# Kernel optimization log

Hardware: AMD Instinct MI355X
Metric: run time of the kernel (lower is better)

The kernel has to match this reference:

```python
import jax, jax.numpy as jnp
import numpy as np
import math

N, CIN, DM, H, W = 4, 64, 32, 64, 64
KH = KW = 3

def setup_inputs() -> dict:
    key = jax.random.key(0)
    ks = jax.random.split(key, 12)
    sc = 0.05
    return {
        "h": jax.random.normal(ks[0], (N, CIN, H, W), jnp.float32),
        "m": jax.random.normal(ks[1], (N, CIN, H, W), jnp.float32),
        "Wh": jax.random.normal(ks[2], (3 * DM, CIN), jnp.float32) * sc,
        "bh": jax.random.normal(ks[3], (3 * DM,), jnp.float32) * sc,
        "Wm": jax.random.normal(ks[4], (2 * DM, CIN), jnp.float32) * sc,
        "bm": jax.random.normal(ks[5], (2 * DM,), jnp.float32) * sc,
        "Wz": jax.random.normal(ks[6], (DM, 2 * DM), jnp.float32) * sc,
        "bz": jax.random.normal(ks[7], (DM,), jnp.float32) * sc,
        "Wo": jax.random.normal(ks[8], (3 * CIN, CIN + DM, KH, KW), jnp.float32) * sc,
        "bo": jax.random.normal(ks[9], (3 * CIN,), jnp.float32) * sc,
    }

def _conv1x1(x, Wt, b):
    # x: [N,Ci,H,W], Wt: [Co,Ci] -> [N,Co,H,W]
    return jnp.einsum('oi,nihw->nohw', Wt, x) + b[None, :, None, None]

def _attend(q, k, v):
    # q,k,v: [N,C,S]; out: [N,C,S]
    C = q.shape[1]
    scores = jnp.einsum('ncs,nct->nst', q, k) / math.sqrt(C)  # [N,S,S]
    attn = jax.nn.softmax(scores, axis=-1)
    return jnp.einsum('nst,nct->ncs', attn, v)

def reference(h, m, Wh, bh, Wm, bm, Wz, bz, Wo, bo):
    n, _, hh, ww = h.shape
    S = hh * ww
    hq, hk, hv = jnp.split(_conv1x1(h, Wh, bh), 3, axis=1)
    mk, mv = jnp.split(_conv1x1(m, Wm, bm), 2, axis=1)
    hq = hq.reshape(n, DM, S)
    hk = hk.reshape(n, DM, S)
    hv = hv.reshape(n, DM, S)
    mk = mk.reshape(n, DM, S)
    mv = mv.reshape(n, DM, S)
    Zh = _attend(hq, hk, hv).reshape(n, DM, hh, ww)
    Zm = _attend(hq, mk, mv).reshape(n, DM, hh, ww)
    Z = _conv1x1(jnp.concatenate([Zh, Zm], axis=1), Wz, bz)
    x = jnp.concatenate([Z, h], axis=1)  # [N, DM+CIN, H, W]
    out = jax.lax.conv_general_dilated(
        x, Wo, window_strides=(1, 1), padding='SAME',
        dimension_numbers=('NCHW', 'OIHW', 'NCHW')) + bo[None, :, None, None]
    i, g, o = jnp.split(out, 3, axis=1)
    i = jax.nn.sigmoid(i)
    g = jnp.tanh(g)
    m_next = i * g + (1.0 - i) * m
    h_next = jax.nn.sigmoid(o) * m_next
    return (h_next, m_next)
```

## Files before the change

### kernel.cpp

```cpp
#include <hip/hip_runtime.h>
#include <math.h>

#define NB 4
#define CIN 64
#define DM 32
#define S 4096
#define NW 8

#define OFF_Q  0
#define OFF_KH 262144
#define OFF_VH 524288
#define OFF_KM 786432
#define OFF_VM 1048576
#define OFF_ZH 1310720
#define OFF_ZM 1572864
#define OFF_WF 1835008

typedef __attribute__((ext_vector_type(8))) short bf16x8;
typedef __attribute__((ext_vector_type(4))) short s16x4;
typedef __attribute__((ext_vector_type(4))) float f32x4;

__device__ inline unsigned short f2b(float x) {
  union { float f; unsigned u; } v;
  v.f = x;
  unsigned r = (v.u + 0x7FFF + ((v.u >> 16) & 1)) >> 16;
  return (unsigned short)r;
}

__device__ inline float b2f(unsigned short u) {
  union { unsigned u; float f; } v;
  v.u = ((unsigned)u) << 16;
  return v.f;
}

__global__ __launch_bounds__(256) void prep_kernel(
    const float* __restrict__ h, const float* __restrict__ m,
    const float* __restrict__ Wh, const float* __restrict__ bh,
    const float* __restrict__ Wm, const float* __restrict__ bm,
    const float* __restrict__ Wo, float* __restrict__ ws) {
  __shared__ float lin[64][64];
  __shared__ unsigned short sm[64][34];
  int bid = blockIdx.x;
  int tid = threadIdx.x;

  if (bid >= 512) {
    int idx = (bid - 512) * 256 + tid;
    int co = idx / 432;
    int rem = idx - co * 432;
    int tap = rem / 48;
    int cp = rem - tap * 48;
    int ci0 = cp * 2;
    float a = Wo[((size_t)co * 96 + ci0) * 9 + tap];
    float b = Wo[((size_t)co * 96 + ci0 + 1) * 9 + tap];
    unsigned val = (unsigned)f2b(a) | ((unsigned)f2b(b) << 16);
    ((unsigned*)(ws + OFF_WF))[idx] = val;
    return;
  }

  int mode = (bid >= 256) ? 1 : 0;
  const float* in = mode ? m : h;
  const float* W = mode ? Wm : Wh;
  const float* b = mode ? bm : bh;
  int lbid = bid & 255;
  int n = lbid >> 6;
  int s0 = (lbid & 63) * 64;
  int sl = tid & 63;
  int cg = tid >> 6;
  const float* inp = in + (size_t)n * CIN * S + s0;
#pragma unroll
  for (int r = 0; r < 16; ++r) {
    int ci = r * 4 + cg;
    lin[ci][sl] = inp[(size_t)ci * S + sl];
  }
  __syncthreads();
  int na = (mode == 0) ? 24 : 16;
  float acc[24];
  for (int k = 0; k < na; ++k) {
    int co = cg + k * 4;
    const float* w = W + co * CIN;
    float a = b[co];
#pragma unroll
    for (int ci = 0; ci < CIN; ++ci) a += w[ci] * lin[ci][sl];
    acc[k] = a;
  }

  unsigned short* qsl = (unsigned short*)(ws + OFF_Q);
  unsigned short* khs = (unsigned short*)(ws + OFF_KH);
  unsigned short* vhs = (unsigned short*)(ws + OFF_VH);
  unsigned short* kms = (unsigned short*)(ws + OFF_KM);
  unsigned short* vms = (unsigned short*)(ws + OFF_VM);

  int ngrp = (mode == 0) ? 2 : 1;
  for (int g = 0; g < ngrp; ++g) {
    __syncthreads();
    const float rs = 0.17677669529663687f;
#pragma unroll
    for (int j = 0; j < 8; ++j) {
      int k = g * 8 + j;
      int c = cg + 4 * j;
      float v = acc[k];
      if (mode == 0 && g == 0) v *= rs;
      sm[sl][c] = f2b(v);
    }
    __syncthreads();
    unsigned short* dst;
    if (mode == 0)
      dst = (g == 0 ? qsl : khs);
    else
      dst = kms;
    unsigned* du = (unsigned*)(dst + ((size_t)n * S + s0) * 32);
#pragma unroll
    for (int i = 0; i < 4; ++i) {
      int idx = tid + i * 256;
      int s = idx >> 4, cp = idx & 15;
      unsigned val = (unsigned)sm[s][2 * cp] | ((unsigned)sm[s][2 * cp + 1] << 16);
      du[idx] = val;
    }
  }
  int k0 = (mode == 0) ? 16 : 8;
  unsigned short* vdst = (mode == 0) ? vhs : vms;
#pragma unroll
  for (int j = 0; j < 8; ++j) {
    int k = k0 + j;
    int c = cg + 4 * j;
    vdst[((size_t)n * DM + c) * S + s0 + sl] = f2b(acc[k]);
  }
}

union AttnSmem {
  unsigned short P[NW][2][16][76];
  struct {
    float osh[NW][2][32][16];
    float lsh[NW][2][16];
    unsigned short Olds[2][16][40];
  } e;
};

__global__ __launch_bounds__(512, 4) void attn_kernel(
    float* __restrict__ ws, const float* __restrict__ Wz,
    const float* __restrict__ bz) {
  __shared__ AttnSmem sm;

  int bid = blockIdx.x;
  int ph = bid & 1;
  int n = (bid >> 1) & 3;
  int q0 = (bid >> 3) * 32;
  int tid = threadIdx.x;
  int w = tid >> 6;
  int lane = tid & 63;
  int ql = lane & 15;
  int quad = lane >> 4;
  int kbase = w * 512;

  const unsigned short* qs = (const unsigned short*)(ws + OFF_Q) + ((size_t)n * S + q0) * 32;
  const unsigned short* Ks = (const unsigned short*)(ws + (ph ? OFF_KM : OFF_KH)) + (size_t)n * S * 32;
  const unsigned short* Vs = (const unsigned short*)(ws + (ph ? OFF_VM : OFF_VH)) + (size_t)n * DM * S;
  unsigned short* Zp = (unsigned short*)(ws + (ph ? OFF_ZM : OFF_ZH)) + (size_t)n * DM * S;

  bf16x8 qf0 = *(const bf16x8*)(qs + ql * 32 + quad * 8);
  bf16x8 qf1 = *(const bf16x8*)(qs + (16 + ql) * 32 + quad * 8);

  f32x4 o00 = {0.f, 0.f, 0.f, 0.f}, o01 = {0.f, 0.f, 0.f, 0.f};
  f32x4 o10 = {0.f, 0.f, 0.f, 0.f}, o11 = {0.f, 0.f, 0.f, 0.f};
  float lrun0 = 0.f, lrun1 = 0.f;
  const f32x4 zinit = {-8.f, -8.f, -8.f, -8.f};

  bf16x8 kf[4], kfn[4], vf[4];
#pragma unroll
  for (int t = 0; t < 4; ++t)
    kf[t] = *(const bf16x8*)(Ks + (size_t)(kbase + t * 16 + ql) * 32 + quad * 8);

  for (int it = 0; it < 8; ++it) {
    int kb = kbase + it * 64;
    int kbn = kbase + ((it + 1) & 7) * 64;
#pragma unroll
    for (int c2 = 0; c2 < 2; ++c2)
#pragma unroll
      for (int t2 = 0; t2 < 2; ++t2)
        vf[c2 * 2 + t2] = *(const bf16x8*)(Vs + (size_t)(t2 * 16 + ql) * S + kb + c2 * 32 + quad * 8);
#pragma unroll
    for (int t = 0; t < 4; ++t)
      kfn[t] = *(const bf16x8*)(Ks + (size_t)(kbn + t * 16 + ql) * 32 + quad * 8);

    float ls0 = 0.f;
#pragma unroll
    for (int t = 0; t < 4; ++t) {
      f32x4 stt = __builtin_amdgcn_mfma_f32_16x16x32_bf16(kf[t], qf0, zinit, 0, 0, 0);
      s16x4 pp;
#pragma unroll
      for (int r = 0; r < 4; ++r) {
        float p = __expf(stt[r]);
        ls0 += p;
        pp[r] = (short)f2b(p);
      }
      *(s16x4*)(&sm.P[w][0][ql][t * 16 + quad * 4]) = pp;
    }
    lrun0 += ls0;
    float ls1 = 0.f;
#pragma unroll
    for (int t = 0; t < 4; ++t) {
      f32x4 stt = __builtin_amdgcn_mfma_f32_16x16x32_bf16(kf[t], qf1, zinit, 0, 0, 0);
      s16x4 pp;
#pragma unroll
      for (int r = 0; r < 4; ++r) {
        float p = __expf(stt[r]);
        ls1 += p;
        pp[r] = (short)f2b(p);
      }
      *(s16x4*)(&sm.P[w][1][ql][t * 16 + quad * 4]) = pp;
    }
    lrun1 += ls1;

    __builtin_amdgcn_s_waitcnt(0xC07F);
    __builtin_amdgcn_wave_barrier();

#pragma unroll
    for (int c2 = 0; c2 < 2; ++c2) {
      bf16x8 pf0 = *(const bf16x8*)(&sm.P[w][0][ql][c2 * 32 + quad * 8]);
      bf16x8 pf1 = *(const bf16x8*)(&sm.P[w][1][ql][c2 * 32 + quad * 8]);
      o00 = __builtin_amdgcn_mfma_f32_16x16x32_bf16(vf[c2 * 2 + 0], pf0, o00, 0, 0, 0);
      o01 = __builtin_amdgcn_mfma_f32_16x16x32_bf16(vf[c2 * 2 + 1], pf0, o01, 0, 0, 0);
      o10 = __builtin_amdgcn_mfma_f32_16x16x32_bf16(vf[c2 * 2 + 0], pf1, o10, 0, 0, 0);
      o11 = __builtin_amdgcn_mfma_f32_16x16x32_bf16(vf[c2 * 2 + 1], pf1, o11, 0, 0, 0);
    }
    __builtin_amdgcn_wave_barrier();

#pragma unroll
    for (int t = 0; t < 4; ++t) kf[t] = kfn[t];
  }

  lrun0 += __shfl_xor(lrun0, 16);
  lrun0 += __shfl_xor(lrun0, 32);
  lrun1 += __shfl_xor(lrun1, 16);
  lrun1 += __shfl_xor(lrun1, 32);

  __syncthreads();
#pragma unroll
  for (int r = 0; r < 4; ++r) {
    sm.e.osh[w][0][quad * 4 + r][ql] = o00[r];
    sm.e.osh[w][0][16 + quad * 4 + r][ql] = o01[r];
    sm.e.osh[w][1][quad * 4 + r][ql] = o10[r];
    sm.e.osh[w][1][16 + quad * 4 + r][ql] = o11[r];
  }
  if (quad == 0) {
    sm.e.lsh[w][0][ql] = lrun0;
    sm.e.lsh[w][1][ql] = lrun1;
  }
  __syncthreads();

  if (w < 2) {
    int qt = w;
    float l = 0.f;
    f32x4 a0 = {0.f, 0.f, 0.f, 0.f}, a1 = {0.f, 0.f, 0.f, 0.f};
#pragma unroll
    for (int i = 0; i < NW; ++i) {
      l += sm.e.lsh[i][qt][ql];
#pragma unroll
      for (int r = 0; r < 4; ++r) {
        a0[r] += sm.e.osh[i][qt][quad * 4 + r][ql];
        a1[r] += sm.e.osh[i][qt][16 + quad * 4 + r][ql];
      }
    }
    float inv = 1.0f / l;
    s16x4 w0, w1;
#pragma unroll
    for (int r = 0; r < 4; ++r) {
      w0[r] = (short)f2b(a0[r] * inv);
      w1[r] = (short)f2b(a1[r] * inv);
    }
    *(s16x4*)(&sm.e.Olds[qt][ql][quad * 4]) = w0;
    *(s16x4*)(&sm.e.Olds[qt][ql][16 + quad * 4]) = w1;
    __builtin_amdgcn_s_waitcnt(0xC07F);
    __builtin_amdgcn_wave_barrier();
    bf16x8 of = *(const bf16x8*)(&sm.e.Olds[qt][ql][quad * 8]);

    const float* wzr0 = Wz + (size_t)ql * (2 * DM) + ph * DM + quad * 8;
    const float* wzr1 = Wz + (size_t)(ql + 16) * (2 * DM) + ph * DM + quad * 8;
    bf16x8 a0f, a1f;
#pragma unroll
    for (int j = 0; j < 8; ++j) {
      a0f[j] = (short)f2b(wzr0[j]);
      a1f[j] = (short)f2b(wzr1[j]);
    }
    f32x4 z0 = {0.f, 0.f, 0.f, 0.f}, z1 = {0.f, 0.f, 0.f, 0.f};
    if (ph == 0) {
#pragma unroll
      for (int r = 0; r < 4; ++r) {
        z0[r] = bz[quad * 4 + r];
        z1[r] = bz[16 + quad * 4 + r];
      }
    }
    z0 = __builtin_amdgcn_mfma_f32_16x16x32_bf16(a0f, of, z0, 0, 0, 0);
    z1 = __builtin_amdgcn_mfma_f32_16x16x32_bf16(a1f, of, z1, 0, 0, 0);
    int qc = q0 + qt * 16 + ql;
#pragma unroll
    for (int r = 0; r < 4; ++r) {
      Zp[(size_t)(quad * 4 + r) * S + qc] = f2b(z0[r]);
      Zp[(size_t)(16 + quad * 4 + r) * S + qc] = f2b(z1[r]);
    }
  }
}

__global__ __launch_bounds__(256) void xsfill_kernel(
    float* __restrict__ ws, const float* __restrict__ h) {
  __shared__ float lin[96][65];
  int bid = blockIdx.x;
  int n = bid >> 6, y = bid & 63;
  int tid = threadIdx.x;
  const unsigned short* Zh = (const unsigned short*)(ws + OFF_ZH) + (size_t)n * DM * S + y * 64;
  const unsigned short* Zm = (const unsigned short*)(ws + OFF_ZM) + (size_t)n * DM * S + y * 64;
  const float* hb = h + ((size_t)n * 64) * S + y * 64;
#pragma unroll
  for (int k = 0; k < 24; ++k) {
    int idx = tid + k * 256;
    int ci = idx >> 6, xx = idx & 63;
    float v;
    if (ci < 32)
      v = b2f(Zh[(size_t)ci * S + xx]) + b2f(Zm[(size_t)ci * S + xx]);
    else
      v = hb[((size_t)(ci - 32)) * S + xx];
    lin[ci][xx] = v;
  }
  __syncthreads();
  unsigned short* rowbase = (unsigned short*)ws + (((size_t)n * 66 + y + 1) * 66) * 96;
  unsigned* xrow = (unsigned*)(rowbase + 96);
#pragma unroll
  for (int k = 0; k < 12; ++k) {
    int u = tid + k * 256;
    int xx = u / 48, cp = u - xx * 48;
    unsigned val = (unsigned)f2b(lin[2 * cp][xx]) | ((unsigned)f2b(lin[2 * cp + 1][xx]) << 16);
    xrow[u] = val;
  }
  if (tid < 96) {
    if (tid < 48)
      ((unsigned*)rowbase)[tid] = 0u;
    else
      ((unsigned*)(rowbase + 65 * 96))[tid - 48] = 0u;
  }
  if (y == 0) {
    unsigned* g = (unsigned*)((unsigned short*)ws + ((size_t)n * 66) * 66 * 96);
    for (int k = 0; k < 13; ++k) {
      int idx = tid + k * 256;
      if (idx < 3168) g[idx] = 0u;
    }
  }
  if (y == 63) {
    unsigned* g = (unsigned*)((unsigned short*)ws + (((size_t)n * 66 + 65) * 66) * 96);
    for (int k = 0; k < 13; ++k) {
      int idx = tid + k * 256;
      if (idx < 3168) g[idx] = 0u;
    }
  }
}

__global__ __launch_bounds__(256) void conv_mfma_kernel(
    const float* __restrict__ ws, const float* __restrict__ m,
    const float* __restrict__ bo, float* __restrict__ out) {
  int bid = blockIdx.x;
  int n = bid >> 7;
  int rem = bid & 127;
  int g = rem & 1;
  int sblk = rem >> 1;
  int tid = threadIdx.x;
  int wv = tid >> 6;
  int lane = tid & 63;
  int ql = lane & 15, quad = lane >> 4;
  int s0 = sblk * 64 + wv * 16;
  int y = s0 >> 6, x0 = s0 & 63;

  const unsigned short* xs = (const unsigned short*)ws;
  const unsigned short* Wf = (const unsigned short*)(ws + OFF_WF);

  f32x4 acc[6];
#pragma unroll
  for (int t = 0; t < 6; ++t) acc[t] = (f32x4){0.f, 0.f, 0.f, 0.f};

  const unsigned short* xb = xs + (((size_t)n * 66 + y) * 66 + (x0 + ql)) * 96 + quad * 8;
  const unsigned short* wb[6];
#pragma unroll
  for (int j = 0; j < 6; ++j) {
    int cob = (j >> 1) * 64 + g * 32 + (j & 1) * 16;
    wb[j] = Wf + (size_t)(cob + ql) * 864 + quad * 8;
  }

#pragma unroll
  for (int dy = 0; dy < 3; ++dy) {
#pragma unroll
    for (int dx = 0; dx < 3; ++dx) {
      int tap = dy * 3 + dx;
      const unsigned short* xp = xb + ((size_t)dy * 66 + dx) * 96;
#pragma unroll
      for (int cc = 0; cc < 3; ++cc) {
        bf16x8 b = *(const bf16x8*)(xp + cc * 32);
        int ko = tap * 96 + cc * 32;
#pragma unroll
        for (int j = 0; j < 6; ++j) {
          bf16x8 wf = *(const bf16x8*)(wb[j] + ko);
          acc[j] = __builtin_amdgcn_mfma_f32_16x16x32_bf16(wf, b, acc[j], 0, 0, 0);
        }
      }
    }
  }

  int s = s0 + ql;
#pragma unroll
  for (int jj = 0; jj < 2; ++jj) {
#pragma unroll
    for (int r = 0; r < 4; ++r) {
      int c = g * 32 + jj * 16 + quad * 4 + r;
      float iv = acc[jj][r] + bo[c];
      float gv = acc[2 + jj][r] + bo[64 + c];
      float ov = acc[4 + jj][r] + bo[128 + c];
      float ig = 1.f / (1.f + __expf(-iv));
      float gg = tanhf(gv);
      float og = 1.f / (1.f + __expf(-ov));
      size_t oidx = (((size_t)n * 64 + c) << 12) + s;
      float mold = m[oidx];
      float mn = ig * gg + (1.f - ig) * mold;
      out[oidx] = og * mn;
      out[(size_t)NB * CIN * S + oidx] = mn;
    }
  }
}

extern "C" void kernel_launch(void* const* d_in, const int* in_sizes, int n_in,
                              void* d_out, int out_size, void* d_ws, size_t ws_size,
                              hipStream_t stream) {
  const float* h = (const float*)d_in[0];
  const float* m = (const float*)d_in[1];
  const float* Wh = (const float*)d_in[2];
  const float* bh = (const float*)d_in[3];
  const float* Wm = (const float*)d_in[4];
  const float* bm = (const float*)d_in[5];
  const float* Wz = (const float*)d_in[6];
  const float* bz = (const float*)d_in[7];
  const float* Wo = (const float*)d_in[8];
  const float* bo = (const float*)d_in[9];
  float* out = (float*)d_out;
  float* ws = (float*)d_ws;

  prep_kernel<<<836, 256, 0, stream>>>(h, m, Wh, bh, Wm, bm, Wo, ws);
  attn_kernel<<<2 * NB * (S / 32), 512, 0, stream>>>(ws, Wz, bz);
  xsfill_kernel<<<NB * 64, 256, 0, stream>>>(ws, h);
  conv_mfma_kernel<<<NB * 128, 256, 0, stream>>>(ws, m, bo, out);
}
```

Measured before the change: 189.1 us.

## Use exp2 softmax, 4-wave attention blocks, register-resident prep inputs

The attention kernel now runs 256-thread blocks with 4 waves, each covering 1024 keys instead of 512. Folding log2(e) into the Q scale and the fixed offset lets it use the hardware exp2 and pack bf16 by truncation through a perm instruction instead of round-to-nearest. The per-tile sums are kept in vector registers and reduced once at the end. The prep kernel loads its 64 input channels straight into registers instead of staging them in LDS and fully unrolls the per-mode projection loops, which raises register pressure and code size. Truncating P to bf16 adds a small rounding bias.

```diff
diff --git a/kernel.cpp b/kernel.cpp
--- a/kernel.cpp
+++ b/kernel.cpp
@@ -5,7 +5,7 @@
 #define CIN 64
 #define DM 32
 #define S 4096
-#define NW 8
+#define NW 4
 
 #define OFF_Q  0
 #define OFF_KH 262144
@@ -19,6 +19,7 @@
 typedef __attribute__((ext_vector_type(8))) short bf16x8;
 typedef __attribute__((ext_vector_type(4))) short s16x4;
 typedef __attribute__((ext_vector_type(4))) float f32x4;
+typedef __attribute__((ext_vector_type(2))) unsigned int u32x2;
 
 __device__ inline unsigned short f2b(float x) {
   union { float f; unsigned u; } v;
@@ -33,12 +34,17 @@
   return v.f;
 }
 
+__device__ inline unsigned fbits(float x) {
+  union { float f; unsigned u; } v;
+  v.f = x;
+  return v.u;
+}
+
 __global__ __launch_bounds__(256) void prep_kernel(
     const float* __restrict__ h, const float* __restrict__ m,
     const float* __restrict__ Wh, const float* __restrict__ bh,
     const float* __restrict__ Wm, const float* __restrict__ bm,
     const float* __restrict__ Wo, float* __restrict__ ws) {
-  __shared__ float lin[64][64];
   __shared__ unsigned short sm[64][34];
   int bid = blockIdx.x;
   int tid = threadIdx.x;
@@ -66,22 +72,33 @@
   int s0 = (lbid & 63) * 64;
   int sl = tid & 63;
   int cg = tid >> 6;
-  const float* inp = in + (size_t)n * CIN * S + s0;
-#pragma unroll
-  for (int r = 0; r < 16; ++r) {
-    int ci = r * 4 + cg;
-    lin[ci][sl] = inp[(size_t)ci * S + sl];
-  }
-  __syncthreads();
-  int na = (mode == 0) ? 24 : 16;
+  const float* inp = in + (size_t)n * CIN * S + s0 + sl;
+
+  float reg[64];
+#pragma unroll
+  for (int ci = 0; ci < 64; ++ci) reg[ci] = inp[(size_t)ci * S];
+
   float acc[24];
-  for (int k = 0; k < na; ++k) {
-    int co = cg + k * 4;
-    const float* w = W + co * CIN;
-    float a = b[co];
-#pragma unroll
-    for (int ci = 0; ci < CIN; ++ci) a += w[ci] * lin[ci][sl];
-    acc[k] = a;
+  if (mode == 0) {
+#pragma unroll
+    for (int k = 0; k < 24; ++k) {
+      int co = cg + k * 4;
+      const float* w = W + co * CIN;
+      float a = b[co];
+#pragma unroll
+      for (int ci = 0; ci < CIN; ++ci) a += w[ci] * reg[ci];
+      acc[k] = a;
+    }
+  } else {
+#pragma unroll
+    for (int k = 0; k < 16; ++k) {
+      int co = cg + k * 4;
+      const float* w = W + co * CIN;
+      float a = b[co];
+#pragma unroll
+      for (int ci = 0; ci < CIN; ++ci) a += w[ci] * reg[ci];
+      acc[k] = a;
+    }
   }
 
   unsigned short* qsl = (unsigned short*)(ws + OFF_Q);
@@ -93,7 +110,7 @@
   int ngrp = (mode == 0) ? 2 : 1;
   for (int g = 0; g < ngrp; ++g) {
     __syncthreads();
-    const float rs = 0.17677669529663687f;
+    const float rs = 0.2550400330665387f;
 #pragma unroll
     for (int j = 0; j < 8; ++j) {
       int k = g * 8 + j;
@@ -128,18 +145,16 @@
 }
 
 union AttnSmem {
-  unsigned short P[NW][2][16][76];
-  struct {
-    float osh[NW][2][32][16];
-    float lsh[NW][2][16];
-    unsigned short Olds[2][16][40];
-  } e;
+  unsigned short P[NW][2][1240];
+  float osh[NW][2][32][16];
 };
 
-__global__ __launch_bounds__(512, 4) void attn_kernel(
+__global__ __launch_bounds__(256, 4) void attn_kernel(
     float* __restrict__ ws, const float* __restrict__ Wz,
     const float* __restrict__ bz) {
   __shared__ AttnSmem sm;
+  __shared__ float lsh[NW][2][16];
+  __shared__ unsigned short Olds[2][16][40];
 
   int bid = blockIdx.x;
   int ph = bid & 1;
@@ -150,7 +165,7 @@
   int lane = tid & 63;
   int ql = lane & 15;
   int quad = lane >> 4;
-  int kbase = w * 512;
+  int kbase = w * 1024;
 
   const unsigned short* qs = (const unsigned short*)(ws + OFF_Q) + ((size_t)n * S + q0) * 32;
   const unsigned short* Ks = (const unsigned short*)(ws + (ph ? OFF_KM : OFF_KH)) + (size_t)n * S * 32;
@@ -162,17 +177,18 @@
 
   f32x4 o00 = {0.f, 0.f, 0.f, 0.f}, o01 = {0.f, 0.f, 0.f, 0.f};
   f32x4 o10 = {0.f, 0.f, 0.f, 0.f}, o11 = {0.f, 0.f, 0.f, 0.f};
-  float lrun0 = 0.f, lrun1 = 0.f;
-  const f32x4 zinit = {-8.f, -8.f, -8.f, -8.f};
+  f32x4 lsv0 = {0.f, 0.f, 0.f, 0.f}, lsv1 = {0.f, 0.f, 0.f, 0.f};
+  const float ZI = -11.541560327111707f;
+  const f32x4 zinit = {ZI, ZI, ZI, ZI};
 
   bf16x8 kf[4], kfn[4], vf[4];
 #pragma unroll
   for (int t = 0; t < 4; ++t)
     kf[t] = *(const bf16x8*)(Ks + (size_t)(kbase + t * 16 + ql) * 32 + quad * 8);
 
-  for (int it = 0; it < 8; ++it) {
+  for (int it = 0; it < 16; ++it) {
     int kb = kbase + it * 64;
-    int kbn = kbase + ((it + 1) & 7) * 64;
+    int kbn = kbase + ((it + 1) & 15) * 64;
 #pragma unroll
     for (int c2 = 0; c2 < 2; ++c2)
 #pragma unroll
@@ -182,42 +198,38 @@
     for (int t = 0; t < 4; ++t)
       kfn[t] = *(const bf16x8*)(Ks + (size_t)(kbn + t * 16 + ql) * 32 + quad * 8);
 
-    float ls0 = 0.f;
 #pragma unroll
     for (int t = 0; t < 4; ++t) {
       f32x4 stt = __builtin_amdgcn_mfma_f32_16x16x32_bf16(kf[t], qf0, zinit, 0, 0, 0);
-      s16x4 pp;
-#pragma unroll
-      for (int r = 0; r < 4; ++r) {
-        float p = __expf(stt[r]);
-        ls0 += p;
-        pp[r] = (short)f2b(p);
-      }
-      *(s16x4*)(&sm.P[w][0][ql][t * 16 + quad * 4]) = pp;
-    }
-    lrun0 += ls0;
-    float ls1 = 0.f;
+      f32x4 e;
+#pragma unroll
+      for (int r = 0; r < 4; ++r) e[r] = __builtin_amdgcn_exp2f(stt[r]);
+      lsv0 += e;
+      u32x2 pk;
+      pk[0] = __builtin_amdgcn_perm(fbits(e[1]), fbits(e[0]), 0x07060302u);
+      pk[1] = __builtin_amdgcn_perm(fbits(e[3]), fbits(e[2]), 0x07060302u);
+      *(u32x2*)(&sm.P[w][0][ql * 76 + t * 16 + quad * 4]) = pk;
+    }
 #pragma unroll
     for (int t = 0; t < 4; ++t) {
       f32x4 stt = __builtin_amdgcn_mfma_f32_16x16x32_bf16(kf[t], qf1, zinit, 0, 0, 0);
-      s16x4 pp;
-#pragma unroll
-      for (int r = 0; r < 4; ++r) {
-        float p = __expf(stt[r]);
-        ls1 += p;
-        pp[r] = (short)f2b(p);
-      }
-      *(s16x4*)(&sm.P[w][1][ql][t * 16 + quad * 4]) = pp;
-    }
-    lrun1 += ls1;
+      f32x4 e;
+#pragma unroll
+      for (int r = 0; r < 4; ++r) e[r] = __builtin_amdgcn_exp2f(stt[r]);
+      lsv1 += e;
+      u32x2 pk;
+      pk[0] = __builtin_amdgcn_perm(fbits(e[1]), fbits(e[0]), 0x07060302u);
+      pk[1] = __builtin_amdgcn_perm(fbits(e[3]), fbits(e[2]), 0x07060302u);
+      *(u32x2*)(&sm.P[w][1][ql * 76 + t * 16 + quad * 4]) = pk;
+    }
 
     __builtin_amdgcn_s_waitcnt(0xC07F);
     __builtin_amdgcn_wave_barrier();
 
 #pragma unroll
     for (int c2 = 0; c2 < 2; ++c2) {
-      bf16x8 pf0 = *(const bf16x8*)(&sm.P[w][0][ql][c2 * 32 + quad * 8]);
-      bf16x8 pf1 = *(const bf16x8*)(&sm.P[w][1][ql][c2 * 32 + quad * 8]);
+      bf16x8 pf0 = *(const bf16x8*)(&sm.P[w][0][ql * 76 + c2 * 32 + quad * 8]);
+      bf16x8 pf1 = *(const bf16x8*)(&sm.P[w][1][ql * 76 + c2 * 32 + quad * 8]);
       o00 = __builtin_amdgcn_mfma_f32_16x16x32_bf16(vf[c2 * 2 + 0], pf0, o00, 0, 0, 0);
       o01 = __builtin_amdgcn_mfma_f32_16x16x32_bf16(vf[c2 * 2 + 1], pf0, o01, 0, 0, 0);
       o10 = __builtin_amdgcn_mfma_f32_16x16x32_bf16(vf[c2 * 2 + 0], pf1, o10, 0, 0, 0);
@@ -229,6 +241,8 @@
     for (int t = 0; t < 4; ++t) kf[t] = kfn[t];
   }
 
+  float lrun0 = lsv0[0] + lsv0[1] + lsv0[2] + lsv0[3];
+  float lrun1 = lsv1[0] + lsv1[1] + lsv1[2] + lsv1[3];
   lrun0 += __shfl_xor(lrun0, 16);
   lrun0 += __shfl_xor(lrun0, 32);
   lrun1 += __shfl_xor(lrun1, 16);
@@ -237,14 +251,14 @@
   __syncthreads();
 #pragma unroll
   for (int r = 0; r < 4; ++r) {
-    sm.e.osh[w][0][quad * 4 + r][ql] = o00[r];
-    sm.e.osh[w][0][16 + quad * 4 + r][ql] = o01[r];
-    sm.e.osh[w][1][quad * 4 + r][ql] = o10[r];
-    sm.e.osh[w][1][16 + quad * 4 + r][ql] = o11[r];
+    sm.osh[w][0][quad * 4 + r][ql] = o00[r];
+    sm.osh[w][0][16 + quad * 4 + r][ql] = o01[r];
+    sm.osh[w][1][quad * 4 + r][ql] = o10[r];
+    sm.osh[w][1][16 + quad * 4 + r][ql] = o11[r];
   }
   if (quad == 0) {
-    sm.e.lsh[w][0][ql] = lrun0;
-    sm.e.lsh[w][1][ql] = lrun1;
+    lsh[w][0][ql] = lrun0;
+    lsh[w][1][ql] = lrun1;
   }
   __syncthreads();
 
@@ -254,11 +268,11 @@
     f32x4 a0 = {0.f, 0.f, 0.f, 0.f}, a1 = {0.f, 0.f, 0.f, 0.f};
 #pragma unroll
     for (int i = 0; i < NW; ++i) {
-      l += sm.e.lsh[i][qt][ql];
+      l += lsh[i][qt][ql];
 #pragma unroll
       for (int r = 0; r < 4; ++r) {
-        a0[r] += sm.e.osh[i][qt][quad * 4 + r][ql];
-        a1[r] += sm.e.osh[i][qt][16 + quad * 4 + r][ql];
+        a0[r] += sm.osh[i][qt][quad * 4 + r][ql];
+        a1[r] += sm.osh[i][qt][16 + quad * 4 + r][ql];
       }
     }
     float inv = 1.0f / l;
@@ -268,11 +282,11 @@
       w0[r] = (short)f2b(a0[r] * inv);
       w1[r] = (short)f2b(a1[r] * inv);
     }
-    *(s16x4*)(&sm.e.Olds[qt][ql][quad * 4]) = w0;
-    *(s16x4*)(&sm.e.Olds[qt][ql][16 + quad * 4]) = w1;
+    *(s16x4*)(&Olds[qt][ql][quad * 4]) = w0;
+    *(s16x4*)(&Olds[qt][ql][16 + quad * 4]) = w1;
     __builtin_amdgcn_s_waitcnt(0xC07F);
     __builtin_amdgcn_wave_barrier();
-    bf16x8 of = *(const bf16x8*)(&sm.e.Olds[qt][ql][quad * 8]);
+    bf16x8 of = *(const bf16x8*)(&Olds[qt][ql][quad * 8]);
 
     const float* wzr0 = Wz + (size_t)ql * (2 * DM) + ph * DM + quad * 8;
     const float* wzr1 = Wz + (size_t)(ql + 16) * (2 * DM) + ph * DM + quad * 8;
@@ -440,7 +454,7 @@
   float* ws = (float*)d_ws;
 
   prep_kernel<<<836, 256, 0, stream>>>(h, m, Wh, bh, Wm, bm, Wo, ws);
-  attn_kernel<<<2 * NB * (S / 32), 512, 0, stream>>>(ws, Wz, bz);
+  attn_kernel<<<2 * NB * (S / 32), 256, 0, stream>>>(ws, Wz, bz);
   xsfill_kernel<<<NB * 64, 256, 0, stream>>>(ws, h);
   conv_mfma_kernel<<<NB * 128, 256, 0, stream>>>(ws, m, bo, out);
 }
```

Result: no change. 186.5 us (-1.4%).
